# Kernel optimization log

Hardware: AMD Instinct MI355X
Metric: run time of the kernel (lower is better)

The kernel has to match this reference:

```python
import jax, jax.numpy as jnp
import numpy as np

EPS = 1e-5
SLOPE = 0.2

def lrelu(x):
    return jnp.where(x > 0, x, SLOPE * x)

def bn_train(x, gamma, beta, axes):
    # training-mode batch norm over `axes`, channel dim = 1 (or features dim for 2D input)
    mean = jnp.mean(x, axis=axes, keepdims=True)
    var = jnp.mean((x - mean) ** 2, axis=axes, keepdims=True)
    sh = [1] * x.ndim
    sh[1] = -1
    return gamma.reshape(sh) * (x - mean) * jax.lax.rsqrt(var + EPS) + beta.reshape(sh)

def knn_sum(x, k):
    # x: (B, C, N). k-NN graph via pairwise squared distance, then sum of
    # gathered neighbor features over the k neighbors -> (B, C, N).
    inner = jnp.einsum('bcn,bcm->bnm', x, x)            # (B,N,N)
    sq = jnp.sum(x * x, axis=1)                          # (B,N)
    neg_dist = 2.0 * inner - sq[:, :, None] - sq[:, None, :]
    _, idx = jax.lax.top_k(neg_dist, k)                  # (B,N,k) nearest (incl. self)
    # gather: feat[b,c,n,j] = x[b,c,idx[b,n,j]]
    feat = jnp.take_along_axis(x[:, :, None, :], idx[:, None, :, :], axis=3)  # (B,C,N,k)
    return jnp.sum(feat, axis=3)

def edge_block(x, W, g, b, k):
    # get_graph_feature -> sum over neighbors -> conv1x1 -> BN -> LeakyReLU
    agg = knn_sum(x, k)                                  # (B,C,N)
    y = jnp.einsum('oc,bcn->bon', W, agg)                # 1x1 conv, no bias
    return lrelu(bn_train(y, g, b, (0, 2)))


def setup_inputs() -> dict:
    key = jax.random.key(0)
    ks = jax.random.split(key, 16)
    B, N, E, OUT = 16, 1024, 1024, 40
    w = lambda k_, sh, s=0.05: jax.random.normal(k_, sh, jnp.float32) * s
    ones = lambda n: jnp.ones((n,), jnp.float32)
    zeros = lambda n: jnp.zeros((n,), jnp.float32)
    return {
        'x': jax.random.normal(ks[0], (B, 3, N), jnp.float32),
        'W1': w(ks[1], (64, 3)),   'g1': ones(64),  'b1': zeros(64),
        'W2': w(ks[2], (64, 64)),  'g2': ones(64),  'b2': zeros(64),
        'W3': w(ks[3], (128, 64)), 'g3': ones(128), 'b3': zeros(128),
        'W4': w(ks[4], (256, 128)),'g4': ones(256), 'b4': zeros(256),
        'W5': w(ks[5], (E, 512)),  'g5': ones(E),   'b5': zeros(E),
        'lin1W': w(ks[6], (512, 2 * E)), 'g6': ones(512), 'b6': zeros(512),
        'lin2W': w(ks[7], (256, 512)), 'lin2b': zeros(256), 'g7': ones(256), 'b7': zeros(256),
        'lin3W': w(ks[8], (OUT, 256)), 'lin3b': zeros(OUT),
        'k': 20,
    }


def reference(x, W1, g1, b1, W2, g2, b2, W3, g3, b3, W4, g4, b4,
              W5, g5, b5, lin1W, g6, b6, lin2W, lin2b, g7, b7,
              lin3W, lin3b, k):
    x1 = edge_block(x,  W1, g1, b1, k)   # (B, 64, N)
    x2 = edge_block(x1, W2, g2, b2, k)   # (B, 64, N)
    x3 = edge_block(x2, W3, g3, b3, k)   # (B,128, N)
    x4 = edge_block(x3, W4, g4, b4, k)   # (B,256, N)
    h = jnp.concatenate([x1, x2, x3, x4], axis=1)        # (B,512,N)
    h = lrelu(bn_train(jnp.einsum('oc,bcn->bon', W5, h), g5, b5, (0, 2)))  # (B,E,N)
    hmax = jnp.max(h, axis=2)
    havg = jnp.mean(h, axis=2)
    z = jnp.concatenate([hmax, havg], axis=1)            # (B, 2E)
    z = lrelu(bn_train(z @ lin1W.T, g6, b6, (0,)))
    z = lrelu(bn_train(z @ lin2W.T + lin2b, g7, b7, (0,)))  # dropout = identity (eval)
    return z @ lin3W.T + lin3b                           # (B, 40)
```

## Files before the change

### kernel.cpp

```cpp
#include <hip/hip_runtime.h>
#include <hip/hip_bf16.h>
#include <math.h>

#define NPTS 1024
#define BATCH 16
#define KNN 20

typedef __attribute__((ext_vector_type(8))) short short8;
typedef __attribute__((ext_vector_type(4))) float f32x4;

__global__ __launch_bounds__(256) void compute_sq_kernel(const float* __restrict__ X,
    long batchStride, int C, float* __restrict__ sq) {
  const int b = blockIdx.y;
  const int m = blockIdx.x * 256 + threadIdx.x;
  const float* Xb = X + (long)b * batchStride;
  float s = 0.f;
  for (int c = 0; c < C; ++c) { float v = Xb[(long)c * NPTS + m]; s += v * v; }
  sq[b * NPTS + m] = s;
}

__global__ __launch_bounds__(256) void transpose_split_kernel(const float* __restrict__ in,
    long inBatchStride, int C, unsigned short* __restrict__ XH,
    unsigned short* __restrict__ XM, unsigned short* __restrict__ XL) {
  __shared__ float tile[64][65];
  const int b  = blockIdx.z;
  const int n0 = blockIdx.x * 64, c0 = blockIdx.y * 64;
  const int tid = threadIdx.x;
  const float* ib = in + (long)b * inBatchStride;
  for (int i = tid; i < 4096; i += 256) {
    int r = i >> 6, cn = i & 63;
    tile[r][cn] = ib[(long)(c0 + r) * NPTS + n0 + cn];
  }
  __syncthreads();
  const long pb = (long)b * ((long)NPTS * C);
  for (int i = tid; i < 4096; i += 256) {
    int r = i >> 6, cc = i & 63;
    float f = tile[cc][r];
    __hip_bfloat16 h = __float2bfloat16(f);
    float r1 = f - __bfloat162float(h);
    __hip_bfloat16 m = __float2bfloat16(r1);
    float r2 = r1 - __bfloat162float(m);
    __hip_bfloat16 l = __float2bfloat16(r2);
    const long o = pb + (long)(n0 + r) * C + c0 + cc;
    XH[o] = *(unsigned short*)&h;
    XM[o] = *(unsigned short*)&m;
    XL[o] = *(unsigned short*)&l;
  }
}

template<int C>
__global__ __launch_bounds__(256) void knn_mfma_kernel(
    const unsigned short* __restrict__ XH, const unsigned short* __restrict__ XM,
    const unsigned short* __restrict__ XL, const float* __restrict__ sqg,
    float* __restrict__ PARTV, unsigned short* __restrict__ PARTI) {
  __shared__ __align__(16) unsigned short QP[6][64][40];
  __shared__ __align__(16) float Dbuf[64][68];
  __shared__ float sqs[256];
  float* region = (float*)&QP[0][0][0];

  const int b     = blockIdx.z;
  const int q0    = blockIdx.x * 64;
  const int p0    = blockIdx.y * 256;
  const int chunk = blockIdx.y;
  const int tid  = threadIdx.x;
  const int lane = tid & 63, w = tid >> 6;
  const int l16  = lane & 15, quad = lane >> 4;
  const int q = lane, sub = w;

  const long plane = (long)b * ((long)NPTS * C);
  const unsigned short* XHb = XH + plane;
  const unsigned short* XMb = XM + plane;
  const unsigned short* XLb = XL + plane;

  sqs[tid] = sqg[b * NPTS + p0 + tid];

  float topv[KNN];
  int   topi[KNN];
  #pragma unroll
  for (int j = 0; j < KNN; ++j) { topv[j] = -INFINITY; topi[j] = 0x7fffffff; }
  float vmin = -INFINITY;

  const int srow = tid >> 2, sseg = (tid & 3) * 8;

  for (int pc = 0; pc < 256; pc += 64) {
    f32x4 acc[4];
    #pragma unroll
    for (int t = 0; t < 4; ++t) acc[t] = (f32x4){0.f, 0.f, 0.f, 0.f};

    for (int kc = 0; kc < C; kc += 32) {
      __syncthreads();
      const long qo = (long)(q0 + srow) * C + kc + sseg;
      const long po = (long)(p0 + pc + srow) * C + kc + sseg;
      *(float4*)&QP[0][srow][sseg] = *(const float4*)&XHb[qo];
      *(float4*)&QP[1][srow][sseg] = *(const float4*)&XMb[qo];
      *(float4*)&QP[2][srow][sseg] = *(const float4*)&XLb[qo];
      *(float4*)&QP[3][srow][sseg] = *(const float4*)&XHb[po];
      *(float4*)&QP[4][srow][sseg] = *(const float4*)&XMb[po];
      *(float4*)&QP[5][srow][sseg] = *(const float4*)&XLb[po];
      __syncthreads();
      const short8 ph = *(const short8*)&QP[3][w * 16 + l16][quad * 8];
      const short8 pm = *(const short8*)&QP[4][w * 16 + l16][quad * 8];
      const short8 pl = *(const short8*)&QP[5][w * 16 + l16][quad * 8];
      #pragma unroll
      for (int t = 0; t < 4; ++t) {
        const short8 qh = *(const short8*)&QP[0][t * 16 + l16][quad * 8];
        const short8 qm = *(const short8*)&QP[1][t * 16 + l16][quad * 8];
        const short8 ql = *(const short8*)&QP[2][t * 16 + l16][quad * 8];
        acc[t] = __builtin_amdgcn_mfma_f32_16x16x32_bf16(ph, qh, acc[t], 0, 0, 0);
        acc[t] = __builtin_amdgcn_mfma_f32_16x16x32_bf16(ph, qm, acc[t], 0, 0, 0);
        acc[t] = __builtin_amdgcn_mfma_f32_16x16x32_bf16(pm, qh, acc[t], 0, 0, 0);
        acc[t] = __builtin_amdgcn_mfma_f32_16x16x32_bf16(pm, qm, acc[t], 0, 0, 0);
        acc[t] = __builtin_amdgcn_mfma_f32_16x16x32_bf16(ph, ql, acc[t], 0, 0, 0);
        acc[t] = __builtin_amdgcn_mfma_f32_16x16x32_bf16(pl, qh, acc[t], 0, 0, 0);
      }
    }
    #pragma unroll
    for (int t = 0; t < 4; ++t)
      #pragma unroll
      for (int r = 0; r < 4; ++r)
        Dbuf[w * 16 + quad * 4 + r][t * 16 + l16] = acc[t][r];
    __syncthreads();

    #pragma unroll 4
    for (int i = 0; i < 16; ++i) {
      const float v = fmaf(2.f, Dbuf[sub * 16 + i][q], -sqs[pc + sub * 16 + i]);
      if (v > vmin) {
        float cv = v; int ci = p0 + pc + sub * 16 + i;
        bool ins = false;
        #pragma unroll
        for (int j = 0; j < KNN; ++j) {
          const float tv = topv[j]; const int ti = topi[j];
          const bool gt = ins || (cv > tv);
          topv[j] = gt ? cv : tv;
          topi[j] = gt ? ci : ti;
          cv = gt ? tv : cv;
          ci = gt ? ti : ci;
          ins = gt;
        }
        vmin = topv[KNN - 1];
      }
    }
  }

  __syncthreads();
  {
    float* mv = region;
    unsigned short* mi = (unsigned short*)(region + 5120);
    const int slot = q * 4 + sub;
    #pragma unroll
    for (int j = 0; j < KNN; ++j) { mv[j * 256 + slot] = topv[j]; mi[j * 256 + slot] = (unsigned short)topi[j]; }
  }
  __syncthreads();
  if (tid < 64) {
    const float* mv = region;
    const unsigned short* mi = (const unsigned short*)(region + 5120);
    int p0_ = 0, p1 = 0, p2 = 0, p3 = 0;
    float* opv = PARTV + (((long)(b * NPTS + q0 + tid)) * 4 + chunk) * KNN;
    unsigned short* opi = PARTI + (((long)(b * NPTS + q0 + tid)) * 4 + chunk) * KNN;
    for (int j = 0; j < KNN; ++j) {
      float bv = -INFINITY; int bi = 0x7fffffff; int bs = 0;
      if (p0_ < KNN) { float v = mv[p0_ * 256 + tid * 4 + 0]; int i = mi[p0_ * 256 + tid * 4 + 0];
        if (v > bv || (v == bv && i < bi)) { bv = v; bi = i; bs = 0; } }
      if (p1 < KNN) { float v = mv[p1 * 256 + tid * 4 + 1]; int i = mi[p1 * 256 + tid * 4 + 1];
        if (v > bv || (v == bv && i < bi)) { bv = v; bi = i; bs = 1; } }
      if (p2 < KNN) { float v = mv[p2 * 256 + tid * 4 + 2]; int i = mi[p2 * 256 + tid * 4 + 2];
        if (v > bv || (v == bv && i < bi)) { bv = v; bi = i; bs = 2; } }
      if (p3 < KNN) { float v = mv[p3 * 256 + tid * 4 + 3]; int i = mi[p3 * 256 + tid * 4 + 3];
        if (v > bv || (v == bv && i < bi)) { bv = v; bi = i; bs = 3; } }
      p0_ += (bs == 0); p1 += (bs == 1); p2 += (bs == 2); p3 += (bs == 3);
      opv[j] = bv; opi[j] = (unsigned short)bi;
    }
  }
}

template<int C>
__global__ __launch_bounds__(256) void knn_kernel(const float* __restrict__ X,
    long batchStride, const float* __restrict__ sqg,
    float* __restrict__ PARTV, unsigned short* __restrict__ PARTI) {
  constexpr int CT = (C < 64) ? C : 64;
  constexpr int REGF = (2 * CT * 64 > 7680) ? 2 * CT * 64 : 7680;
  __shared__ float Dbuf[64][68];
  __shared__ float region[REGF];

  float* qbuf = region;
  float* pbuf = region + CT * 64;

  const int b     = blockIdx.z;
  const int q0    = blockIdx.x * 64;
  const int p0    = blockIdx.y * 256;
  const int chunk = blockIdx.y;
  const int tid = threadIdx.x;
  const int ty  = tid >> 4, tx = tid & 15;
  const int q   = tid & 63;
  const int sub = tid >> 6;
  const float* Xb = X + (long)b * batchStride;
  const float* sqb = sqg + b * NPTS;

  float topv[KNN];
  int   topi[KNN];
  #pragma unroll
  for (int j = 0; j < KNN; ++j) { topv[j] = -INFINITY; topi[j] = 0x7fffffff; }
  float vmin = -INFINITY;

  for (int pc = p0; pc < p0 + 256; pc += 64) {
    float acc[4][4] = {};
    for (int cc = 0; cc < C; cc += CT) {
      __syncthreads();
      for (int t = tid; t < 64 * CT; t += 256) {
        int c = t >> 6, m = t & 63;
        qbuf[c * 64 + m] = Xb[(long)(cc + c) * NPTS + q0 + m];
        pbuf[c * 64 + m] = Xb[(long)(cc + c) * NPTS + pc + m];
      }
      __syncthreads();
      #pragma unroll
      for (int c = 0; c < CT; ++c) {
        const float4 qv = *(const float4*)&qbuf[c * 64 + ty * 4];
        const float4 pv = *(const float4*)&pbuf[c * 64 + tx * 4];
        acc[0][0] += qv.x * pv.x; acc[0][1] += qv.x * pv.y; acc[0][2] += qv.x * pv.z; acc[0][3] += qv.x * pv.w;
        acc[1][0] += qv.y * pv.x; acc[1][1] += qv.y * pv.y; acc[1][2] += qv.y * pv.z; acc[1][3] += qv.y * pv.w;
        acc[2][0] += qv.z * pv.x; acc[2][1] += qv.z * pv.y; acc[2][2] += qv.z * pv.z; acc[2][3] += qv.z * pv.w;
        acc[3][0] += qv.w * pv.x; acc[3][1] += qv.w * pv.y; acc[3][2] += qv.w * pv.z; acc[3][3] += qv.w * pv.w;
      }
    }
    #pragma unroll
    for (int j = 0; j < 4; ++j) {
      const int p = pc + tx * 4 + j;
      const float sq = sqb[p];
      float4 dv;
      dv.x = 2.f * acc[0][j] - sq;
      dv.y = 2.f * acc[1][j] - sq;
      dv.z = 2.f * acc[2][j] - sq;
      dv.w = 2.f * acc[3][j] - sq;
      *(float4*)&Dbuf[tx * 4 + j][ty * 4] = dv;
    }
    __syncthreads();

    #pragma unroll 4
    for (int i = 0; i < 16; ++i) {
      const float v = Dbuf[sub * 16 + i][q];
      if (v > vmin) {
        float cv = v; int ci = pc + sub * 16 + i;
        bool ins = false;
        #pragma unroll
        for (int j = 0; j < KNN; ++j) {
          const float tv = topv[j]; const int ti = topi[j];
          const bool gt = ins || (cv > tv);
          topv[j] = gt ? cv : tv;
          topi[j] = gt ? ci : ti;
          cv = gt ? tv : cv;
          ci = gt ? ti : ci;
          ins = gt;
        }
        vmin = topv[KNN - 1];
      }
    }
  }

  __syncthreads();
  {
    float* mv = region;
    unsigned short* mi = (unsigned short*)(region + 5120);
    const int slot = q * 4 + sub;
    #pragma unroll
    for (int j = 0; j < KNN; ++j) { mv[j * 256 + slot] = topv[j]; mi[j * 256 + slot] = (unsigned short)topi[j]; }
  }
  __syncthreads();
  if (tid < 64) {
    const float* mv = region;
    const unsigned short* mi = (const unsigned short*)(region + 5120);
    int p0_ = 0, p1 = 0, p2 = 0, p3 = 0;
    float* opv = PARTV + (((long)(b * NPTS + q0 + tid)) * 4 + chunk) * KNN;
    unsigned short* opi = PARTI + (((long)(b * NPTS + q0 + tid)) * 4 + chunk) * KNN;
    for (int j = 0; j < KNN; ++j) {
      float bv = -INFINITY; int bi = 0x7fffffff; int bs = 0;
      if (p0_ < KNN) { float v = mv[p0_ * 256 + tid * 4 + 0]; int i = mi[p0_ * 256 + tid * 4 + 0];
        if (v > bv || (v == bv && i < bi)) { bv = v; bi = i; bs = 0; } }
      if (p1 < KNN) { float v = mv[p1 * 256 + tid * 4 + 1]; int i = mi[p1 * 256 + tid * 4 + 1];
        if (v > bv || (v == bv && i < bi)) { bv = v; bi = i; bs = 1; } }
      if (p2 < KNN) { float v = mv[p2 * 256 + tid * 4 + 2]; int i = mi[p2 * 256 + tid * 4 + 2];
        if (v > bv || (v == bv && i < bi)) { bv = v; bi = i; bs = 2; } }
      if (p3 < KNN) { float v = mv[p3 * 256 + tid * 4 + 3]; int i = mi[p3 * 256 + tid * 4 + 3];
        if (v > bv || (v == bv && i < bi)) { bv = v; bi = i; bs = 3; } }
      p0_ += (bs == 0); p1 += (bs == 1); p2 += (bs == 2); p3 += (bs == 3);
      opv[j] = bv; opi[j] = (unsigned short)bi;
    }
  }
}

__global__ __launch_bounds__(256) void knn_merge_kernel(const float* __restrict__ PARTV,
    const unsigned short* __restrict__ PARTI, int* __restrict__ idxOut) {
  const int idx = blockIdx.x * 256 + threadIdx.x;
  const float* pv = PARTV + (long)idx * 4 * KNN;
  const unsigned short* pi = PARTI + (long)idx * 4 * KNN;
  int p0 = 0, p1 = 0, p2 = 0, p3 = 0;
  int* op = idxOut + (long)idx * KNN;
  for (int j = 0; j < KNN; ++j) {
    float bv = -INFINITY; int bi = 0x7fffffff; int bs = 0;
    if (p0 < KNN) { float v = pv[0 * KNN + p0]; int i = pi[0 * KNN + p0];
      if (v > bv || (v == bv && i < bi)) { bv = v; bi = i; bs = 0; } }
    if (p1 < KNN) { float v = pv[1 * KNN + p1]; int i = pi[1 * KNN + p1];
      if (v > bv || (v == bv && i < bi)) { bv = v; bi = i; bs = 1; } }
    if (p2 < KNN) { float v = pv[2 * KNN + p2]; int i = pi[2 * KNN + p2];
      if (v > bv || (v == bv && i < bi)) { bv = v; bi = i; bs = 2; } }
    if (p3 < KNN) { float v = pv[3 * KNN + p3]; int i = pi[3 * KNN + p3];
      if (v > bv || (v == bv && i < bi)) { bv = v; bi = i; bs = 3; } }
    p0 += (bs == 0); p1 += (bs == 1); p2 += (bs == 2); p3 += (bs == 3);
    op[j] = bi;
  }
}

__global__ __launch_bounds__(256) void gather_sum_kernel(const float* __restrict__ X,
    long batchStride, int C, const int* __restrict__ idx, float* __restrict__ agg) {
  __shared__ int sidx[256][KNN + 1];
  const int b     = blockIdx.z;
  const int n0    = blockIdx.x * 256;
  const int cbase = blockIdx.y * 8;
  const int tid   = threadIdx.x;
  const int* ib = idx + ((long)(b * NPTS + n0)) * KNN;
  for (int t = tid; t < 256 * KNN; t += 256) {
    sidx[t / KNN][t % KNN] = ib[t];
  }
  __syncthreads();
  const float* Xb = X + (long)b * batchStride;
  float* ab = agg + (long)b * C * NPTS;
  const int cend = min(cbase + 8, C);
  for (int c = cbase; c < cend; ++c) {
    const float* row = Xb + (long)c * NPTS;
    float s = 0.f;
    #pragma unroll
    for (int j = 0; j < KNN; ++j) s += row[sidx[tid][j]];
    ab[(long)c * NPTS + n0 + tid] = s;
  }
}

__global__ __launch_bounds__(256) void conv_kernel(const float* __restrict__ Xin, long inBatchStride,
    const float* __restrict__ W, int C, int O,
    float* __restrict__ Yout, long outBatchStride, int outChanOffset) {
  __shared__ float Wt[32][68];
  __shared__ float Xt[32][68];
  const int b   = blockIdx.z;
  const int o0  = blockIdx.y * 64;
  const int n0  = blockIdx.x * 64;
  const int tid = threadIdx.x;
  const int ty  = tid >> 4, tx = tid & 15;
  const float* Xb = Xin + (long)b * inBatchStride;
  float acc[4][4] = {};
  for (int cc = 0; cc < C; cc += 32) {
    const int cw = min(32, C - cc);
    __syncthreads();
    for (int t = tid; t < 64 * 32; t += 256) {
      int oo = t >> 5, kk = t & 31;
      Wt[kk][oo] = (kk < cw) ? W[(long)(o0 + oo) * C + cc + kk] : 0.f;
    }
    for (int t = tid; t < 32 * 64; t += 256) {
      int kk = t >> 6, nn = t & 63;
      Xt[kk][nn] = (kk < cw) ? Xb[(long)(cc + kk) * NPTS + n0 + nn] : 0.f;
    }
    __syncthreads();
    #pragma unroll
    for (int kk = 0; kk < 32; ++kk) {
      const float4 wv = *(const float4*)&Wt[kk][ty * 4];
      const float4 xv = *(const float4*)&Xt[kk][tx * 4];
      acc[0][0] += wv.x * xv.x; acc[0][1] += wv.x * xv.y; acc[0][2] += wv.x * xv.z; acc[0][3] += wv.x * xv.w;
      acc[1][0] += wv.y * xv.x; acc[1][1] += wv.y * xv.y; acc[1][2] += wv.y * xv.z; acc[1][3] += wv.y * xv.w;
      acc[2][0] += wv.z * xv.x; acc[2][1] += wv.z * xv.y; acc[2][2] += wv.z * xv.z; acc[2][3] += wv.z * xv.w;
      acc[3][0] += wv.w * xv.x; acc[3][1] += wv.w * xv.y; acc[3][2] += wv.w * xv.z; acc[3][3] += wv.w * xv.w;
    }
  }
  #pragma unroll
  for (int i = 0; i < 4; ++i) {
    float4 v = make_float4(acc[i][0], acc[i][1], acc[i][2], acc[i][3]);
    *(float4*)&Yout[(long)b * outBatchStride + (long)(outChanOffset + o0 + ty * 4 + i) * NPTS + n0 + tx * 4] = v;
  }
}

__global__ __launch_bounds__(256) void transpose_bf16_kernel(const float* __restrict__ in,
    long inBatchStride, int C, unsigned short* __restrict__ outT) {
  __shared__ float tile[64][65];
  const int b  = blockIdx.z;
  const int n0 = blockIdx.x * 64, c0 = blockIdx.y * 64;
  const int tid = threadIdx.x;
  const float* ib = in + (long)b * inBatchStride;
  for (int i = tid; i < 4096; i += 256) {
    int r = i >> 6, cn = i & 63;
    tile[r][cn] = ib[(long)(c0 + r) * NPTS + n0 + cn];
  }
  __syncthreads();
  unsigned short* ob = outT + (long)b * ((long)NPTS * C);
  for (int i = tid; i < 4096; i += 256) {
    int r = i >> 6, cc = i & 63;
    __hip_bfloat16 h = __float2bfloat16(tile[cc][r]);
    ob[(long)(n0 + r) * C + c0 + cc] = *(unsigned short*)&h;
  }
}

__global__ void convert_bf16_kernel(const float* __restrict__ in,
                                    unsigned short* __restrict__ out, int n) {
  int i = blockIdx.x * 256 + threadIdx.x;
  if (i < n) { __hip_bfloat16 h = __float2bfloat16(in[i]); out[i] = *(unsigned short*)&h; }
}

__global__ __launch_bounds__(256) void conv_mfma_kernel(const unsigned short* __restrict__ Wbf,
    const unsigned short* __restrict__ XT, int C,
    float* __restrict__ Yout, long outBatchStride, int outChanOffset) {
  __shared__ unsigned short Wl[128][40];
  __shared__ unsigned short Xl[128][40];
  const int b  = blockIdx.z;
  const int o0 = blockIdx.y * 128;
  const int n0 = blockIdx.x * 128;
  const int tid  = threadIdx.x;
  const int lane = tid & 63, wid = tid >> 6;
  const int wo = (wid >> 1) * 64, wn = (wid & 1) * 64;
  const int l16 = lane & 15, quad = lane >> 4;
  const unsigned short* Wg = Wbf + (long)o0 * C;
  const unsigned short* Xg = XT + (long)b * ((long)NPTS * C) + (long)n0 * C;

  f32x4 acc[4][4];
  #pragma unroll
  for (int i = 0; i < 4; ++i)
    #pragma unroll
    for (int j = 0; j < 4; ++j) acc[i][j] = (f32x4){0.f, 0.f, 0.f, 0.f};

  for (int kk = 0; kk < C; kk += 32) {
    __syncthreads();
    #pragma unroll
    for (int it = 0; it < 2; ++it) {
      const int id = tid + it * 256;
      const int r = id >> 2, qq = id & 3;
      const float4 va = *(const float4*)&Wg[(long)r * C + kk + qq * 8];
      const float4 vb = *(const float4*)&Xg[(long)r * C + kk + qq * 8];
      *(float4*)&Wl[r][qq * 8] = va;
      *(float4*)&Xl[r][qq * 8] = vb;
    }
    __syncthreads();
    short8 af[4], bfr[4];
    #pragma unroll
    for (int i = 0; i < 4; ++i) af[i]  = *(const short8*)&Wl[wo + i * 16 + l16][quad * 8];
    #pragma unroll
    for (int j = 0; j < 4; ++j) bfr[j] = *(const short8*)&Xl[wn + j * 16 + l16][quad * 8];
    #pragma unroll
    for (int i = 0; i < 4; ++i)
      #pragma unroll
      for (int j = 0; j < 4; ++j)
        acc[i][j] = __builtin_amdgcn_mfma_f32_16x16x32_bf16(af[i], bfr[j], acc[i][j], 0, 0, 0);
  }

  float* Yb = Yout + (long)b * outBatchStride + (long)outChanOffset * NPTS;
  #pragma unroll
  for (int i = 0; i < 4; ++i) {
    #pragma unroll
    for (int r = 0; r < 4; ++r) {
      const int o = o0 + wo + i * 16 + quad * 4 + r;
      float* row = Yb + (long)o * NPTS + n0 + wn;
      #pragma unroll
      for (int j = 0; j < 4; ++j) row[j * 16 + l16] = acc[i][j][r];
    }
  }
}

__global__ __launch_bounds__(256) void bn_stats_kernel(const float* __restrict__ Y, long batchStride,
    int chanOffset, float* __restrict__ meanOut, float* __restrict__ rstdOut) {
  const int o   = blockIdx.x;
  const int tid = threadIdx.x;
  const float* base = Y + (long)(chanOffset + o) * NPTS;
  float s = 0.f, s2 = 0.f;
  for (int b = 0; b < BATCH; ++b) {
    const float* p = base + (long)b * batchStride;
    for (int t = tid; t < NPTS; t += 256) { float v = p[t]; s += v; s2 += v * v; }
  }
  for (int off = 32; off > 0; off >>= 1) { s += __shfl_down(s, off); s2 += __shfl_down(s2, off); }
  __shared__ float r1[4], r2[4];
  const int wid = tid >> 6;
  if ((tid & 63) == 0) { r1[wid] = s; r2[wid] = s2; }
  __syncthreads();
  if (tid == 0) {
    s  = r1[0] + r1[1] + r1[2] + r1[3];
    s2 = r2[0] + r2[1] + r2[2] + r2[3];
    float m   = s * (1.f / 16384.f);
    float var = s2 * (1.f / 16384.f) - m * m;
    meanOut[o] = m;
    rstdOut[o] = rsqrtf(var + 1e-5f);
  }
}

__global__ __launch_bounds__(256) void bn_apply_kernel(float* __restrict__ Y, long batchStride, int chanOffset,
    const float* __restrict__ meanB, const float* __restrict__ rstdB,
    const float* __restrict__ g, const float* __restrict__ beta) {
  const int n = blockIdx.x * 256 + threadIdx.x;
  const int o = blockIdx.y;
  const int b = blockIdx.z;
  float* p = Y + (long)b * batchStride + (long)(chanOffset + o) * NPTS;
  const float sc = rstdB[o] * g[o];
  float v = (p[n] - meanB[o]) * sc + beta[o];
  p[n] = (v > 0.f) ? v : 0.2f * v;
}

__global__ __launch_bounds__(256) void bn_pool_kernel(const float* __restrict__ H,
    const float* __restrict__ meanB, const float* __restrict__ rstdB,
    const float* __restrict__ g, const float* __restrict__ beta,
    float* __restrict__ Z) {
  const int o   = blockIdx.x;
  const int b   = blockIdx.y;
  const int tid = threadIdx.x;
  const float* p = H + (long)b * (1024L * NPTS) + (long)o * NPTS;
  const float sc = rstdB[o] * g[o], mu = meanB[o], bb = beta[o];
  float mx = -INFINITY, s = 0.f;
  for (int t = tid; t < NPTS; t += 256) {
    float v = (p[t] - mu) * sc + bb;
    v = (v > 0.f) ? v : 0.2f * v;
    mx = fmaxf(mx, v);
    s += v;
  }
  for (int off = 32; off > 0; off >>= 1) { mx = fmaxf(mx, __shfl_down(mx, off)); s += __shfl_down(s, off); }
  __shared__ float rm[4], rs[4];
  const int wid = tid >> 6;
  if ((tid & 63) == 0) { rm[wid] = mx; rs[wid] = s; }
  __syncthreads();
  if (tid == 0) {
    mx = fmaxf(fmaxf(rm[0], rm[1]), fmaxf(rm[2], rm[3]));
    s  = rs[0] + rs[1] + rs[2] + rs[3];
    Z[(long)b * 2048 + o]        = mx;
    Z[(long)b * 2048 + 1024 + o] = s * (1.f / 1024.f);
  }
}

__global__ __launch_bounds__(256) void fc_wave_kernel(const float* __restrict__ in,
    const float* __restrict__ Wm, const float* __restrict__ bias,
    float* __restrict__ out, int Cin, int Oout) {
  const int wid  = threadIdx.x >> 6;
  const int lane = threadIdx.x & 63;
  const int o = blockIdx.x * 4 + wid;
  if (o >= Oout) return;
  const float* wp = Wm + (long)o * Cin;
  float acc[BATCH];
  #pragma unroll
  for (int b = 0; b < BATCH; ++b) acc[b] = 0.f;
  for (int c = lane; c < Cin; c += 64) {
    const float w = wp[c];
    #pragma unroll
    for (int b = 0; b < BATCH; ++b) acc[b] += w * in[b * Cin + c];
  }
  #pragma unroll
  for (int b = 0; b < BATCH; ++b) {
    #pragma unroll
    for (int off = 32; off > 0; off >>= 1) acc[b] += __shfl_down(acc[b], off);
  }
  if (lane == 0) {
    const float bs = bias ? bias[o] : 0.f;
    #pragma unroll
    for (int b = 0; b < BATCH; ++b) out[b * Oout + o] = acc[b] + bs;
  }
}

__global__ void bn_small_kernel(float* __restrict__ buf, const float* __restrict__ g,
    const float* __restrict__ beta, int O) {
  const int o = blockIdx.x * 256 + threadIdx.x;
  if (o >= O) return;
  float s = 0.f, s2 = 0.f;
  for (int b = 0; b < BATCH; ++b) { float v = buf[b * O + o]; s += v; s2 += v * v; }
  const float m   = s * (1.f / 16.f);
  const float var = s2 * (1.f / 16.f) - m * m;
  const float sc  = rsqrtf(var + 1e-5f) * g[o];
  const float bb  = beta[o];
  for (int b = 0; b < BATCH; ++b) {
    float v = (buf[b * O + o] - m) * sc + bb;
    buf[b * O + o] = (v > 0.f) ? v : 0.2f * v;
  }
}

extern "C" void kernel_launch(void* const* d_in, const int* in_sizes, int n_in,
                              void* d_out, int out_size, void* d_ws, size_t ws_size,
                              hipStream_t stream) {
  const float* x   = (const float*)d_in[0];
  const float* W1  = (const float*)d_in[1];
  const float* g1  = (const float*)d_in[2];
  const float* b1  = (const float*)d_in[3];
  const float* W2  = (const float*)d_in[4];
  const float* g2  = (const float*)d_in[5];
  const float* b2  = (const float*)d_in[6];
  const float* W3  = (const float*)d_in[7];
  const float* g3  = (const float*)d_in[8];
  const float* b3  = (const float*)d_in[9];
  const float* W4  = (const float*)d_in[10];
  const float* g4  = (const float*)d_in[11];
  const float* b4  = (const float*)d_in[12];
  const float* W5  = (const float*)d_in[13];
  const float* g5  = (const float*)d_in[14];
  const float* b5  = (const float*)d_in[15];
  const float* l1W = (const float*)d_in[16];
  const float* g6  = (const float*)d_in[17];
  const float* b6  = (const float*)d_in[18];
  const float* l2W = (const float*)d_in[19];
  const float* l2b = (const float*)d_in[20];
  const float* g7  = (const float*)d_in[21];
  const float* b7  = (const float*)d_in[22];
  const float* l3W = (const float*)d_in[23];
  const float* l3b = (const float*)d_in[24];

  float* ws   = (float*)d_ws;
  float* Xcat = ws;
  float* H    = Xcat + 8388608;
  float* REG  = H + 16777216;
  float* AGG  = REG;
  unsigned short* AGGT = (unsigned short*)(REG + 2097152);
  unsigned short* XbfT = (unsigned short*)REG;
  int*   IDX  = (int*)(REG + 4194304);
  float* MEAN = (float*)(IDX + 327680);
  float* RSTD = MEAN + 1024;
  float* Z    = RSTD + 1024;
  float* Z1   = Z + 32768;
  float* Z2   = Z1 + 8192;
  unsigned short* W4bf = (unsigned short*)(Z2 + 4096);
  unsigned short* W5bf = W4bf + 32768;

  float* SQ    = H;
  float* PARTV = H + 16384;
  unsigned short* PARTI = (unsigned short*)(PARTV + 1310720);
  unsigned short* XH = (unsigned short*)(H + 1982464);
  unsigned short* XM = (unsigned short*)(H + 1982464 + 1048576);
  unsigned short* XL = (unsigned short*)(H + 1982464 + 2097152);

  const long XS = 512L * 1024;
  const long HS = 1024L * 1024;
  const dim3 knnGrid(16, 4, 16);

  compute_sq_kernel<<<dim3(4, 16), 256, 0, stream>>>(x, 3L * 1024, 3, SQ);
  knn_kernel<3><<<knnGrid, 256, 0, stream>>>(x, 3L * 1024, SQ, PARTV, PARTI);
  knn_merge_kernel<<<64, 256, 0, stream>>>(PARTV, PARTI, IDX);
  gather_sum_kernel<<<dim3(4, 1, 16), 256, 0, stream>>>(x, 3L * 1024, 3, IDX, AGG);
  conv_kernel<<<dim3(16, 1, 16), 256, 0, stream>>>(AGG, 3L * 1024, W1, 3, 64, Xcat, XS, 0);
  bn_stats_kernel<<<64, 256, 0, stream>>>(Xcat, XS, 0, MEAN, RSTD);
  bn_apply_kernel<<<dim3(4, 64, 16), 256, 0, stream>>>(Xcat, XS, 0, MEAN, RSTD, g1, b1);

  compute_sq_kernel<<<dim3(4, 16), 256, 0, stream>>>(Xcat, XS, 64, SQ);
  transpose_split_kernel<<<dim3(16, 1, 16), 256, 0, stream>>>(Xcat, XS, 64, XH, XM, XL);
  knn_mfma_kernel<64><<<knnGrid, 256, 0, stream>>>(XH, XM, XL, SQ, PARTV, PARTI);
  knn_merge_kernel<<<64, 256, 0, stream>>>(PARTV, PARTI, IDX);
  gather_sum_kernel<<<dim3(4, 8, 16), 256, 0, stream>>>(Xcat, XS, 64, IDX, AGG);
  conv_kernel<<<dim3(16, 1, 16), 256, 0, stream>>>(AGG, 64L * 1024, W2, 64, 64, Xcat, XS, 64);
  bn_stats_kernel<<<64, 256, 0, stream>>>(Xcat, XS, 64, MEAN, RSTD);
  bn_apply_kernel<<<dim3(4, 64, 16), 256, 0, stream>>>(Xcat, XS, 64, MEAN, RSTD, g2, b2);

  compute_sq_kernel<<<dim3(4, 16), 256, 0, stream>>>(Xcat + 64L * 1024, XS, 64, SQ);
  transpose_split_kernel<<<dim3(16, 1, 16), 256, 0, stream>>>(Xcat + 64L * 1024, XS, 64, XH, XM, XL);
  knn_mfma_kernel<64><<<knnGrid, 256, 0, stream>>>(XH, XM, XL, SQ, PARTV, PARTI);
  knn_merge_kernel<<<64, 256, 0, stream>>>(PARTV, PARTI, IDX);
  gather_sum_kernel<<<dim3(4, 8, 16), 256, 0, stream>>>(Xcat + 64L * 1024, XS, 64, IDX, AGG);
  conv_kernel<<<dim3(16, 2, 16), 256, 0, stream>>>(AGG, 64L * 1024, W3, 64, 128, Xcat, XS, 128);
  bn_stats_kernel<<<128, 256, 0, stream>>>(Xcat, XS, 128, MEAN, RSTD);
  bn_apply_kernel<<<dim3(4, 128, 16), 256, 0, stream>>>(Xcat, XS, 128, MEAN, RSTD, g3, b3);

  compute_sq_kernel<<<dim3(4, 16), 256, 0, stream>>>(Xcat + 128L * 1024, XS, 128, SQ);
  transpose_split_kernel<<<dim3(16, 2, 16), 256, 0, stream>>>(Xcat + 128L * 1024, XS, 128, XH, XM, XL);
  knn_mfma_kernel<128><<<knnGrid, 256, 0, stream>>>(XH, XM, XL, SQ, PARTV, PARTI);
  knn_merge_kernel<<<64, 256, 0, stream>>>(PARTV, PARTI, IDX);
  gather_sum_kernel<<<dim3(4, 16, 16), 256, 0, stream>>>(Xcat + 128L * 1024, XS, 128, IDX, AGG);
  convert_bf16_kernel<<<128, 256, 0, stream>>>(W4, W4bf, 256 * 128);
  transpose_bf16_kernel<<<dim3(16, 2, 16), 256, 0, stream>>>(AGG, 128L * 1024, 128, AGGT);
  conv_mfma_kernel<<<dim3(8, 2, 16), 256, 0, stream>>>(W4bf, AGGT, 128, Xcat, XS, 256);
  bn_stats_kernel<<<256, 256, 0, stream>>>(Xcat, XS, 256, MEAN, RSTD);
  bn_apply_kernel<<<dim3(4, 256, 16), 256, 0, stream>>>(Xcat, XS, 256, MEAN, RSTD, g4, b4);

  convert_bf16_kernel<<<2048, 256, 0, stream>>>(W5, W5bf, 1024 * 512);
  transpose_bf16_kernel<<<dim3(16, 8, 16), 256, 0, stream>>>(Xcat, XS, 512, XbfT);
  conv_mfma_kernel<<<dim3(8, 8, 16), 256, 0, stream>>>(W5bf, XbfT, 512, H, HS, 0);
  bn_stats_kernel<<<1024, 256, 0, stream>>>(H, HS, 0, MEAN, RSTD);
  bn_pool_kernel<<<dim3(1024, 16), 256, 0, stream>>>(H, MEAN, RSTD, g5, b5, Z);

  fc_wave_kernel<<<128, 256, 0, stream>>>(Z, l1W, nullptr, Z1, 2048, 512);
  bn_small_kernel<<<2, 256, 0, stream>>>(Z1, g6, b6, 512);
  fc_wave_kernel<<<64, 256, 0, stream>>>(Z1, l2W, l2b, Z2, 512, 256);
  bn_small_kernel<<<1, 256, 0, stream>>>(Z2, g7, b7, 256);
  fc_wave_kernel<<<10, 256, 0, stream>>>(Z2, l3W, l3b, (float*)d_out, 256, 40);
}
```

Before: 1.054 ms.

## Prefetch kNN tiles into registers, fold distance epilogue, vectorize neighbor gather

The kNN MFMA kernel now prefetches the next global tile into registers while it computes on the current shared-memory tile, which hides global load latency. It also applies the 2*dot - sq epilogue in registers before writing Dbuf, so the sqs shared array goes away. The transpose kernel additionally writes a point-major fp32 copy, and a new gather kernel reads 8 contiguous channels per neighbor with float4 loads instead of scattered per-channel reads. The cost is extra register pressure, an extra fp32 transposed buffer write, and more scratch memory.

```diff
diff --git a/kernel.cpp b/kernel.cpp
--- a/kernel.cpp
+++ b/kernel.cpp
@@ -21,7 +21,8 @@
 
 __global__ __launch_bounds__(256) void transpose_split_kernel(const float* __restrict__ in,
     long inBatchStride, int C, unsigned short* __restrict__ XH,
-    unsigned short* __restrict__ XM, unsigned short* __restrict__ XL) {
+    unsigned short* __restrict__ XM, unsigned short* __restrict__ XL,
+    float* __restrict__ XT) {
   __shared__ float tile[64][65];
   const int b  = blockIdx.z;
   const int n0 = blockIdx.x * 64, c0 = blockIdx.y * 64;
@@ -45,6 +46,7 @@
     XH[o] = *(unsigned short*)&h;
     XM[o] = *(unsigned short*)&m;
     XL[o] = *(unsigned short*)&l;
+    XT[o] = f;
   }
 }
 
@@ -55,7 +57,6 @@
     float* __restrict__ PARTV, unsigned short* __restrict__ PARTI) {
   __shared__ __align__(16) unsigned short QP[6][64][40];
   __shared__ __align__(16) float Dbuf[64][68];
-  __shared__ float sqs[256];
   float* region = (float*)&QP[0][0][0];
 
   const int b     = blockIdx.z;
@@ -72,7 +73,12 @@
   const unsigned short* XMb = XM + plane;
   const unsigned short* XLb = XL + plane;
 
-  sqs[tid] = sqg[b * NPTS + p0 + tid];
+  float sqw[4][4];
+  #pragma unroll
+  for (int pci = 0; pci < 4; ++pci)
+    #pragma unroll
+    for (int r = 0; r < 4; ++r)
+      sqw[pci][r] = sqg[b * NPTS + p0 + pci * 64 + w * 16 + quad * 4 + r];
 
   float topv[KNN];
   int   topi[KNN];
@@ -81,23 +87,46 @@
   float vmin = -INFINITY;
 
   const int srow = tid >> 2, sseg = (tid & 3) * 8;
-
-  for (int pc = 0; pc < 256; pc += 64) {
+  constexpr int KCN = C / 32;
+
+  float4 rg0, rg1, rg2, rg3, rg4, rg5;
+  {
+    const long qo = (long)(q0 + srow) * C + sseg;
+    const long po = (long)(p0 + srow) * C + sseg;
+    rg0 = *(const float4*)&XHb[qo];
+    rg1 = *(const float4*)&XMb[qo];
+    rg2 = *(const float4*)&XLb[qo];
+    rg3 = *(const float4*)&XHb[po];
+    rg4 = *(const float4*)&XMb[po];
+    rg5 = *(const float4*)&XLb[po];
+  }
+
+  for (int pci = 0; pci < 4; ++pci) {
     f32x4 acc[4];
     #pragma unroll
     for (int t = 0; t < 4; ++t) acc[t] = (f32x4){0.f, 0.f, 0.f, 0.f};
 
-    for (int kc = 0; kc < C; kc += 32) {
+    for (int kci = 0; kci < KCN; ++kci) {
       __syncthreads();
-      const long qo = (long)(q0 + srow) * C + kc + sseg;
-      const long po = (long)(p0 + pc + srow) * C + kc + sseg;
-      *(float4*)&QP[0][srow][sseg] = *(const float4*)&XHb[qo];
-      *(float4*)&QP[1][srow][sseg] = *(const float4*)&XMb[qo];
-      *(float4*)&QP[2][srow][sseg] = *(const float4*)&XLb[qo];
-      *(float4*)&QP[3][srow][sseg] = *(const float4*)&XHb[po];
-      *(float4*)&QP[4][srow][sseg] = *(const float4*)&XMb[po];
-      *(float4*)&QP[5][srow][sseg] = *(const float4*)&XLb[po];
+      *(float4*)&QP[0][srow][sseg] = rg0;
+      *(float4*)&QP[1][srow][sseg] = rg1;
+      *(float4*)&QP[2][srow][sseg] = rg2;
+      *(float4*)&QP[3][srow][sseg] = rg3;
+      *(float4*)&QP[4][srow][sseg] = rg4;
+      *(float4*)&QP[5][srow][sseg] = rg5;
       __syncthreads();
+      const int ns = pci * KCN + kci + 1;
+      if (ns < 4 * KCN) {
+        const int npc = ns / KCN, nkc = (ns % KCN) * 32;
+        const long qo = (long)(q0 + srow) * C + nkc + sseg;
+        const long po = (long)(p0 + npc * 64 + srow) * C + nkc + sseg;
+        rg0 = *(const float4*)&XHb[qo];
+        rg1 = *(const float4*)&XMb[qo];
+        rg2 = *(const float4*)&XLb[qo];
+        rg3 = *(const float4*)&XHb[po];
+        rg4 = *(const float4*)&XMb[po];
+        rg5 = *(const float4*)&XLb[po];
+      }
       const short8 ph = *(const short8*)&QP[3][w * 16 + l16][quad * 8];
       const short8 pm = *(const short8*)&QP[4][w * 16 + l16][quad * 8];
       const short8 pl = *(const short8*)&QP[5][w * 16 + l16][quad * 8];
@@ -118,14 +147,14 @@
     for (int t = 0; t < 4; ++t)
       #pragma unroll
       for (int r = 0; r < 4; ++r)
-        Dbuf[w * 16 + quad * 4 + r][t * 16 + l16] = acc[t][r];
+        Dbuf[w * 16 + quad * 4 + r][t * 16 + l16] = fmaf(2.f, acc[t][r], -sqw[pci][r]);
     __syncthreads();
 
     #pragma unroll 4
     for (int i = 0; i < 16; ++i) {
-      const float v = fmaf(2.f, Dbuf[sub * 16 + i][q], -sqs[pc + sub * 16 + i]);
+      const float v = Dbuf[sub * 16 + i][q];
       if (v > vmin) {
-        float cv = v; int ci = p0 + pc + sub * 16 + i;
+        float cv = v; int ci = p0 + pci * 64 + sub * 16 + i;
         bool ins = false;
         #pragma unroll
         for (int j = 0; j < KNN; ++j) {
@@ -330,6 +359,37 @@
     #pragma unroll
     for (int j = 0; j < KNN; ++j) s += row[sidx[tid][j]];
     ab[(long)c * NPTS + n0 + tid] = s;
+  }
+}
+
+__global__ __launch_bounds__(256) void gather_sum_vec_kernel(const float* __restrict__ XT,
+    int C, const int* __restrict__ idx, float* __restrict__ agg) {
+  __shared__ int sidx[256][KNN + 1];
+  const int b     = blockIdx.z;
+  const int n0    = blockIdx.x * 256;
+  const int cbase = blockIdx.y * 16;
+  const int tid   = threadIdx.x;
+  const int* ib = idx + ((long)(b * NPTS + n0)) * KNN;
+  for (int t = tid; t < 256 * KNN; t += 256) {
+    sidx[t / KNN][t % KNN] = ib[t];
+  }
+  __syncthreads();
+  const float* Xb = XT + (long)b * ((long)NPTS * C);
+  float* ab = agg + (long)b * C * NPTS;
+  const int cend = min(cbase + 16, C);
+  for (int c = cbase; c < cend; c += 8) {
+    float a0 = 0.f, a1 = 0.f, a2 = 0.f, a3 = 0.f, a4 = 0.f, a5 = 0.f, a6 = 0.f, a7 = 0.f;
+    #pragma unroll
+    for (int j = 0; j < KNN; ++j) {
+      const float* rp = Xb + (long)sidx[tid][j] * C + c;
+      const float4 v0 = *(const float4*)rp;
+      const float4 v1 = *(const float4*)(rp + 4);
+      a0 += v0.x; a1 += v0.y; a2 += v0.z; a3 += v0.w;
+      a4 += v1.x; a5 += v1.y; a6 += v1.z; a7 += v1.w;
+    }
+    float* op = ab + (long)c * NPTS + n0 + tid;
+    op[0 * NPTS] = a0; op[1 * NPTS] = a1; op[2 * NPTS] = a2; op[3 * NPTS] = a3;
+    op[4 * NPTS] = a4; op[5 * NPTS] = a5; op[6 * NPTS] = a6; op[7 * NPTS] = a7;
   }
 }
 
@@ -619,6 +679,7 @@
   unsigned short* XH = (unsigned short*)(H + 1982464);
   unsigned short* XM = (unsigned short*)(H + 1982464 + 1048576);
   unsigned short* XL = (unsigned short*)(H + 1982464 + 2097152);
+  float* XTf = H + 1982464 + 3145728;
 
   const long XS = 512L * 1024;
   const long HS = 1024L * 1024;
@@ -633,28 +694,28 @@
   bn_apply_kernel<<<dim3(4, 64, 16), 256, 0, stream>>>(Xcat, XS, 0, MEAN, RSTD, g1, b1);
 
   compute_sq_kernel<<<dim3(4, 16), 256, 0, stream>>>(Xcat, XS, 64, SQ);
-  transpose_split_kernel<<<dim3(16, 1, 16), 256, 0, stream>>>(Xcat, XS, 64, XH, XM, XL);
+  transpose_split_kernel<<<dim3(16, 1, 16), 256, 0, stream>>>(Xcat, XS, 64, XH, XM, XL, XTf);
   knn_mfma_kernel<64><<<knnGrid, 256, 0, stream>>>(XH, XM, XL, SQ, PARTV, PARTI);
   knn_merge_kernel<<<64, 256, 0, stream>>>(PARTV, PARTI, IDX);
-  gather_sum_kernel<<<dim3(4, 8, 16), 256, 0, stream>>>(Xcat, XS, 64, IDX, AGG);
+  gather_sum_vec_kernel<<<dim3(4, 4, 16), 256, 0, stream>>>(XTf, 64, IDX, AGG);
   conv_kernel<<<dim3(16, 1, 16), 256, 0, stream>>>(AGG, 64L * 1024, W2, 64, 64, Xcat, XS, 64);
   bn_stats_kernel<<<64, 256, 0, stream>>>(Xcat, XS, 64, MEAN, RSTD);
   bn_apply_kernel<<<dim3(4, 64, 16), 256, 0, stream>>>(Xcat, XS, 64, MEAN, RSTD, g2, b2);
 
   compute_sq_kernel<<<dim3(4, 16), 256, 0, stream>>>(Xcat + 64L * 1024, XS, 64, SQ);
-  transpose_split_kernel<<<dim3(16, 1, 16), 256, 0, stream>>>(Xcat + 64L * 1024, XS, 64, XH, XM, XL);
+  transpose_split_kernel<<<dim3(16, 1, 16), 256, 0, stream>>>(Xcat + 64L * 1024, XS, 64, XH, XM, XL, XTf);
   knn_mfma_kernel<64><<<knnGrid, 256, 0, stream>>>(XH, XM, XL, SQ, PARTV, PARTI);
   knn_merge_kernel<<<64, 256, 0, stream>>>(PARTV, PARTI, IDX);
-  gather_sum_kernel<<<dim3(4, 8, 16), 256, 0, stream>>>(Xcat + 64L * 1024, XS, 64, IDX, AGG);
+  gather_sum_vec_kernel<<<dim3(4, 4, 16), 256, 0, stream>>>(XTf, 64, IDX, AGG);
   conv_kernel<<<dim3(16, 2, 16), 256, 0, stream>>>(AGG, 64L * 1024, W3, 64, 128, Xcat, XS, 128);
   bn_stats_kernel<<<128, 256, 0, stream>>>(Xcat, XS, 128, MEAN, RSTD);
   bn_apply_kernel<<<dim3(4, 128, 16), 256, 0, stream>>>(Xcat, XS, 128, MEAN, RSTD, g3, b3);
 
   compute_sq_kernel<<<dim3(4, 16), 256, 0, stream>>>(Xcat + 128L * 1024, XS, 128, SQ);
-  transpose_split_kernel<<<dim3(16, 2, 16), 256, 0, stream>>>(Xcat + 128L * 1024, XS, 128, XH, XM, XL);
+  transpose_split_kernel<<<dim3(16, 2, 16), 256, 0, stream>>>(Xcat + 128L * 1024, XS, 128, XH, XM, XL, XTf);
   knn_mfma_kernel<128><<<knnGrid, 256, 0, stream>>>(XH, XM, XL, SQ, PARTV, PARTI);
   knn_merge_kernel<<<64, 256, 0, stream>>>(PARTV, PARTI, IDX);
-  gather_sum_kernel<<<dim3(4, 16, 16), 256, 0, stream>>>(Xcat + 128L * 1024, XS, 128, IDX, AGG);
+  gather_sum_vec_kernel<<<dim3(4, 8, 16), 256, 0, stream>>>(XTf, 128, IDX, AGG);
   convert_bf16_kernel<<<128, 256, 0, stream>>>(W4, W4bf, 256 * 128);
   transpose_bf16_kernel<<<dim3(16, 2, 16), 256, 0, stream>>>(AGG, 128L * 1024, 128, AGGT);
   conv_mfma_kernel<<<dim3(8, 2, 16), 256, 0, stream>>>(W4bf, AGGT, 128, Xcat, XS, 256);
```

Result: faster. 1.025 ms (median of 3 runs) (-2.7%).
